# Kernel tuning notes

Measured on AMD Instinct MI355X. Metric: run time of the kernel, lower is better.

Reference implementation:

```python
import jax, jax.numpy as jnp
import numpy as np

DIM, DFF, NH = 768, 2048, 12
HD = DIM // NH
N, NOBJ, L = 16, 52, 24
EPS = 1e-5


def setup_inputs() -> dict:
    key = jax.random.key(0)
    ks = jax.random.split(key, 16)
    g = lambda k, shape: jax.random.normal(k, shape, jnp.float32) * 0.02
    inp = {
        "lang": jax.random.normal(ks[0], (N, L, DIM), jnp.float32),
        "obj": jax.random.normal(ks[1], (N, NOBJ, DIM), jnp.float32),
        "lang_mask": jnp.ones((N, L), jnp.int32),
        "obj_mask": jnp.ones((N, NOBJ), jnp.int32),
        "co_mask": jnp.ones((N, L, NOBJ), jnp.int32),
    }
    # two multi-head attention blocks (edge / node): q,k,v,o projections
    for i, nm in enumerate(["e_wq", "e_wk", "e_wv", "e_wo", "n_wq", "n_wk", "n_wv", "n_wo"]):
        inp[nm] = g(ks[2 + i], (DIM, DIM))
        inp[nm.replace("w", "b")] = jnp.zeros((DIM,), jnp.float32)
    inp["ffn_w1"] = g(ks[10], (2 * DIM, DFF)); inp["ffn_b1"] = jnp.zeros((DFF,), jnp.float32)
    inp["ffn_w2"] = g(ks[11], (DFF, DIM)); inp["ffn_b2"] = jnp.zeros((DIM,), jnp.float32)
    for nm in ["ln_e", "ln_q", "ln2"]:
        inp[nm + "_g"] = jnp.ones((DIM,), jnp.float32)
        inp[nm + "_b"] = jnp.zeros((DIM,), jnp.float32)
    return inp


def _layernorm(x, g, b):
    m = jnp.mean(x, -1, keepdims=True)
    v = jnp.mean((x - m) ** 2, -1, keepdims=True)
    return (x - m) * jax.lax.rsqrt(v + EPS) * g + b


def _fwd(lang, obj, co_mask,
         e_wq, e_bq, e_wk, e_bk, e_wv, e_bv, e_wo, e_bo,
         n_wq, n_bq, n_wk, n_bk, n_wv, n_bv, n_wo, n_bo,
         ffn_w1, ffn_b1, ffn_w2, ffn_b2,
         ln_e_g, ln_e_b, ln_q_g, ln_q_b, ln2_g, ln2_b):
    scale = jnp.float32(1.0 / np.sqrt(HD))
    co_t = co_mask.swapaxes(1, 2)  # [N, nobj, L]: query objects attend over lang keys

    # ---- node branch: standard cross-attention obj -> lang ----
    qh = (obj @ n_wq + n_bq).reshape(N, NOBJ, NH, HD)
    kh = (lang @ n_wk + n_bk).reshape(N, L, NH, HD)
    vh = (lang @ n_wv + n_bv).reshape(N, L, NH, HD)
    s = jnp.einsum('nqhd,nlhd->nhql', qh, kh) * scale  # [N,H,nobj,L]
    s = jnp.where(co_t[:, None, :, :] > 0, s, jnp.float32(-1e9))
    a = jax.nn.softmax(s, axis=-1)
    node = jnp.einsum('nhql,nlhd->nqhd', a, vh).reshape(N, NOBJ, DIM) @ n_wo + n_bo

    # ---- edge branch: pairwise diffs attend over lang, then max over partner ----
    diff = obj[:, :, None, :] - obj[:, None, :, :]            # [N,i,j,D]
    qhe = (diff @ e_wq + e_bq).reshape(N, NOBJ, NOBJ, NH, HD)
    khe = (lang @ e_wk + e_bk).reshape(N, L, NH, HD)
    vhe = (lang @ e_wv + e_bv).reshape(N, L, NH, HD)
    se = jnp.einsum('nijhd,nlhd->nhijl', qhe, khe) * scale    # [N,H,i,j,L]
    # mask depends on (n, j, l): torch repeats co_mask^T over the i batch dim
    se = jnp.where(co_t[:, None, None, :, :] > 0, se, jnp.float32(-1e9))
    ae = jax.nn.softmax(se, axis=-1)
    oe = jnp.einsum('nhijl,nlhd->nijhd', ae, vhe).reshape(N, NOBJ, NOBJ, DIM)
    oe = oe @ e_wo + e_bo                                      # [N,i,j,D]
    edge = jnp.max(oe, axis=2)                                 # max over query/partner j -> [N,i,D]

    # ---- fuse ----
    xe = _layernorm(obj + edge, ln_e_g, ln_e_b)
    xn = _layernorm(obj + node, ln_q_g, ln_q_b)
    h = jnp.concatenate((xn, xe), -1)
    h = jax.nn.relu(h @ ffn_w1 + ffn_b1) @ ffn_w2 + ffn_b2
    return _layernorm(xn + h, ln2_g, ln2_b)


def reference(lang, obj, lang_mask, obj_mask, co_mask,
              e_wq, e_bq, e_wk, e_bk, e_wv, e_bv, e_wo, e_bo,
              n_wq, n_bq, n_wk, n_bk, n_wv, n_bv, n_wo, n_bo,
              ffn_w1, ffn_b1, ffn_w2, ffn_b2,
              ln_e_g, ln_e_b, ln_q_g, ln_q_b, ln2_g, ln2_b):
    return _fwd(lang, obj, co_mask,
                e_wq, e_bq, e_wk, e_bk, e_wv, e_bv, e_wo, e_bo,
                n_wq, n_bq, n_wk, n_bk, n_wv, n_bv, n_wo, n_bo,
                ffn_w1, ffn_b1, ffn_w2, ffn_b2,
                ln_e_g, ln_e_b, ln_q_g, ln_q_b, ln2_g, ln2_b)
```

## Files before the change

kernel.cpp:

```cpp
#include <hip/hip_runtime.h>
#include <math.h>

#define NOBJ 52
#define LL 24
#define NHEAD 12

typedef __attribute__((ext_vector_type(8))) short bf16x8;
typedef __attribute__((ext_vector_type(4))) float f32x4;
typedef __attribute__((ext_vector_type(4))) unsigned int u32x4;
typedef __attribute__((ext_vector_type(2))) unsigned int u32x2;

__device__ __forceinline__ unsigned short f2b(float x) {
    union { float f; unsigned int u; } v; v.f = x;
    unsigned int r = v.u + 0x7fffu + ((v.u >> 16) & 1u);
    return (unsigned short)(r >> 16);
}
__device__ __forceinline__ float b2f(unsigned short u) {
    union { unsigned int u; float f; } v; v.u = ((unsigned int)u) << 16;
    return v.f;
}
__device__ __forceinline__ unsigned int pack2(float a, float b) {
    return (unsigned int)f2b(a) | ((unsigned int)f2b(b) << 16);
}
__device__ __forceinline__ f32x4 mfma16(bf16x8 a, bf16x8 b, f32x4 c) {
    return __builtin_amdgcn_mfma_f32_16x16x32_bf16(a, b, c, 0, 0, 0);
}
__device__ __forceinline__ void gl_lds16(const void* g, void* lds) {
    __builtin_amdgcn_global_load_lds(
        (const __attribute__((address_space(1))) unsigned int*)g,
        (__attribute__((address_space(3))) unsigned int*)lds, 16, 0, 0);
}

__device__ __forceinline__ void transpose_tile(const float* __restrict__ src,
    unsigned short* __restrict__ dst, int K, int N, int t, char* smem)
{
    float (*ts)[65] = (float(*)[65])smem;
    const int tid = threadIdx.x;
    const int ntk = K >> 6;
    const int k0 = (t % ntk) << 6, n0 = (t / ntk) << 6;
    const int tx = tid & 63, ty = tid >> 6;
    #pragma unroll
    for (int i2 = 0; i2 < 16; ++i2) {
        const int row = i2 * 4 + ty;
        ts[row][tx] = src[(size_t)(k0 + row) * N + n0 + tx];
    }
    __syncthreads();
    #pragma unroll
    for (int i2 = 0; i2 < 16; ++i2) {
        const int row = i2 * 4 + ty;
        dst[(size_t)(n0 + row) * K + k0 + tx] = f2b(ts[tx][row]);
    }
}

__global__ __launch_bounds__(256)
void pack_all_kernel(const float* s0, const float* s1, const float* s2,
                     const float* s3, const float* s4, const float* s5,
                     const float* s6, const float* s7,
                     const float* s8, const float* s9,
                     unsigned short* d0, unsigned short* d1, unsigned short* d2,
                     unsigned short* d3, unsigned short* d4, unsigned short* d5,
                     unsigned short* d6, unsigned short* d7,
                     unsigned short* d8, unsigned short* d9,
                     const float* obj, const float* lang, const float* n_bq,
                     const float* e_bk, const float* e_bv,
                     const float* n_bk, const float* n_bv,
                     unsigned short* objb, unsigned short* langb,
                     float* bqc, float* blc)
{
    __shared__ __align__(16) char smem[16640];
    const int bid = blockIdx.x;
    const int tid = threadIdx.x;
    if (bid < 2304) {
        const float* src; unsigned short* dst; int K, N, t;
        if (bid < 1152) {
            const int job = bid / 144; t = bid % 144; K = 768; N = 768;
            switch (job) {
                case 0: src = s0; dst = d0; break;
                case 1: src = s1; dst = d1; break;
                case 2: src = s2; dst = d2; break;
                case 3: src = s3; dst = d3; break;
                case 4: src = s4; dst = d4; break;
                case 5: src = s5; dst = d5; break;
                case 6: src = s6; dst = d6; break;
                default: src = s7; dst = d7; break;
            }
        } else if (bid < 1920) { t = bid - 1152; K = 1536; N = 2048; src = s8; dst = d8; }
        else                   { t = bid - 1920; K = 2048; N = 768;  src = s9; dst = d9; }
        transpose_tile(src, dst, K, N, t, smem);
    } else {
        const int base = ((bid - 2304) * 256 + tid) * 4;
        const int T0 = 638976, T1 = 933888, T2 = 935424, T3 = 938496;
        if (base >= T3) return;
        if (base < T0) {
            f32x4 v = *(const f32x4*)(obj + base);
            *(u32x2*)(objb + base) = (u32x2){pack2(v[0], v[1]), pack2(v[2], v[3])};
        } else if (base < T1) {
            const int j = base - T0;
            f32x4 v = *(const f32x4*)(lang + j);
            *(u32x2*)(langb + j) = (u32x2){pack2(v[0], v[1]), pack2(v[2], v[3])};
        } else if (base < T2) {
            const int j = base - T1;
            if (j < 768) { *(f32x4*)(bqc + j) = (f32x4){0.f, 0.f, 0.f, 0.f}; }
            else         { *(f32x4*)(bqc + j) = *(const f32x4*)(n_bq + j - 768); }
        } else {
            const int j = base - T2;
            const int s = j / 768, c = j % 768;
            const float* p = (s == 0) ? e_bk : (s == 1) ? e_bv : (s == 2) ? n_bk : n_bv;
            *(f32x4*)(blc + j) = *(const f32x4*)(p + c);
        }
    }
}

struct GemmJob {
    const unsigned short* A; const unsigned short* Bt; const float* bias;
    float* C; unsigned short* Cb;
    int lda, ldc, K, nbx, nb, relu, swz;
};

__device__ __forceinline__ void gemm_body(const GemmJob J, int bid, char* smem)
{
    unsigned short* As = (unsigned short*)smem;
    unsigned short* Bs = (unsigned short*)(smem + 16384);
    int bx, by;
    if (J.swz) {
        const int cpx = J.nb >> 3;
        const int gid = (bid & 7) * cpx + (bid >> 3);
        const int nbm = J.nb / J.nbx;
        bx = gid / nbm; by = gid % nbm;
    } else { bx = bid % J.nbx; by = bid / J.nbx; }
    const int n0 = bx * 128, m0 = by * 64;
    const int tid = threadIdx.x;
    const int lane = tid & 63;
    const int w = tid >> 6, wr = w >> 1, wc = w & 1;
    const int lr = lane & 15, lk = lane >> 4;
    const int lda = J.lda, K = J.K;
    const unsigned short* Ab = J.A + (size_t)m0 * lda;
    const unsigned short* Bb = J.Bt + (size_t)n0 * K;

    f32x4 acc[2][4] = {};
    const int NT = K >> 6;

    #pragma unroll
    for (int q = 0; q < 2; ++q) {
        const int c = q * 256 + tid, row = c >> 3, p = (c & 7) ^ (row & 7);
        gl_lds16(Ab + (size_t)row * lda + p * 8, As + c * 8);
    }
    #pragma unroll
    for (int q = 0; q < 4; ++q) {
        const int c = q * 256 + tid, row = c >> 3, p = (c & 7) ^ (row & 7);
        gl_lds16(Bb + (size_t)row * K + p * 8, Bs + c * 8);
    }
    __syncthreads();

    for (int t = 0; t < NT; ++t) {
        const int cur = t & 1;
        if (t + 1 < NT) {
            const int k0 = (t + 1) << 6;
            #pragma unroll
            for (int q = 0; q < 2; ++q) {
                const int c = q * 256 + tid, row = c >> 3, p = (c & 7) ^ (row & 7);
                gl_lds16(Ab + (size_t)row * lda + k0 + p * 8, As + (cur ^ 1) * 4096 + c * 8);
            }
            #pragma unroll
            for (int q = 0; q < 4; ++q) {
                const int c = q * 256 + tid, row = c >> 3, p = (c & 7) ^ (row & 7);
                gl_lds16(Bb + (size_t)row * K + k0 + p * 8, Bs + (cur ^ 1) * 8192 + c * 8);
            }
        }
        #pragma unroll
        for (int kk = 0; kk < 2; ++kk) {
            bf16x8 af[2], bv[4];
            #pragma unroll
            for (int mt = 0; mt < 2; ++mt) {
                const int row = wr * 32 + mt * 16 + lr;
                const int pc = (kk * 4 + lk) ^ (row & 7);
                af[mt] = *(const bf16x8*)(As + cur * 4096 + row * 64 + pc * 8);
            }
            #pragma unroll
            for (int nt = 0; nt < 4; ++nt) {
                const int col = wc * 64 + nt * 16 + lr;
                const int pc = (kk * 4 + lk) ^ (col & 7);
                bv[nt] = *(const bf16x8*)(Bs + cur * 8192 + col * 64 + pc * 8);
            }
            #pragma unroll
            for (int mt = 0; mt < 2; ++mt)
                #pragma unroll
                for (int nt = 0; nt < 4; ++nt)
                    acc[mt][nt] = mfma16(af[mt], bv[nt], acc[mt][nt]);
        }
        __syncthreads();
    }

    #pragma unroll
    for (int mt = 0; mt < 2; ++mt) {
        #pragma unroll
        for (int nt = 0; nt < 4; ++nt) {
            const int col = n0 + wc * 64 + nt * 16 + lr;
            const float bvv = J.bias ? J.bias[col] : 0.f;
            #pragma unroll
            for (int r = 0; r < 4; ++r) {
                const int row = m0 + wr * 32 + mt * 16 + lk * 4 + r;
                float v = acc[mt][nt][r] + bvv;
                if (J.relu) v = fmaxf(v, 0.f);
                if (J.C)  J.C[(size_t)row * J.ldc + col] = v;
                if (J.Cb) J.Cb[(size_t)row * J.ldc + col] = f2b(v);
            }
        }
    }
}

__global__ __launch_bounds__(256)
void gemm_tn(GemmJob j0, GemmJob j1)
{
    __shared__ __align__(16) char smem[49152];
    const int bid = blockIdx.x;
    if (bid < j0.nb) gemm_body(j0, bid, smem);
    else gemm_body(j1, bid - j0.nb, smem);
}

__global__ __launch_bounds__(256)
void mid3_kernel(const unsigned short* __restrict__ QCb,
                 const unsigned short* __restrict__ LCb,
                 const unsigned short* __restrict__ Wet,
                 const unsigned short* __restrict__ Wot,
                 const float* __restrict__ e_bq,
                 unsigned short* __restrict__ VWe,
                 unsigned short* __restrict__ VWn,
                 float* __restrict__ S2e, float* __restrict__ Tb,
                 float* __restrict__ S2n)
{
    __shared__ __align__(16) union USm {
        struct { unsigned short As[8192], Bs[8192]; } g;
        unsigned short Ct[128 * 136];
        struct { float sA[52][68], sB[24][68]; } s;
    } U;
    const int bid = blockIdx.x;
    const int tid = threadIdx.x;

    if (bid < 432) {
        const int sub = bid >= 216;
        const int b = sub ? bid - 216 : bid;
        const int aoff = sub ? 2304 : 768;
        const unsigned short* Bt = sub ? Wot : Wet;
        unsigned short* Vout = sub ? VWn : VWe;

        const int h = b / 18, rm = b % 18, mt = rm / 6, ntile = rm % 6;
        const int m0 = mt * 128, n0 = ntile * 128;
        const int lane = tid & 63, w = tid >> 6, wr = w >> 1, wc = w & 1;
        const int lr = lane & 15, lk = lane >> 4;
        #pragma unroll
        for (int q = 0; q < 4; ++q) {
            const int c = q * 256 + tid, row = c >> 3, p = (c & 7) ^ (row & 7);
            gl_lds16(LCb + (size_t)(m0 + row) * 3072 + aoff + h * 64 + p * 8, &U.g.As[c * 8]);
            gl_lds16(Bt + (size_t)(n0 + row) * 768 + h * 64 + p * 8, &U.g.Bs[c * 8]);
        }
        __syncthreads();
        f32x4 acc[4][4] = {};
        #pragma unroll
        for (int kk = 0; kk < 2; ++kk) {
            bf16x8 af[4], bv[4];
            #pragma unroll
            for (int m2 = 0; m2 < 4; ++m2) {
                const int row = wr * 64 + m2 * 16 + lr;
                const int pc = (kk * 4 + lk) ^ (row & 7);
                af[m2] = *(const bf16x8*)&U.g.As[row * 64 + pc * 8];
            }
            #pragma unroll
            for (int n2 = 0; n2 < 4; ++n2) {
                const int col = wc * 64 + n2 * 16 + lr;
                const int pc = (kk * 4 + lk) ^ (col & 7);
                bv[n2] = *(const bf16x8*)&U.g.Bs[col * 64 + pc * 8];
            }
            #pragma unroll
            for (int m2 = 0; m2 < 4; ++m2)
                #pragma unroll
                for (int n2 = 0; n2 < 4; ++n2)
                    acc[m2][n2] = mfma16(af[m2], bv[n2], acc[m2][n2]);
        }
        __syncthreads();
        #pragma unroll
        for (int m2 = 0; m2 < 4; ++m2)
            #pragma unroll
            for (int n2 = 0; n2 < 4; ++n2) {
                const int col = wc * 64 + n2 * 16 + lr;
                #pragma unroll
                for (int r = 0; r < 4; ++r) {
                    const int row = wr * 64 + m2 * 16 + lk * 4 + r;
                    U.Ct[row * 136 + col] = f2b(acc[m2][n2][r]);
                }
            }
        __syncthreads();
        #pragma unroll
        for (int q = 0; q < 8; ++q) {
            const int item = q * 256 + tid;
            const int dl = item & 127, kg = item >> 7;
            const int m = m0 + kg * 8;
            const int nn = m / 24, l0 = m % 24;
            const int kc = (h * 24 + l0) >> 3;
            const int ks = kc >> 2;
            const int dg = n0 + dl;
            const int kpos = (kc & 3) ^ ((dg >> 1) & 3);
            u32x4 uu;
            #pragma unroll
            for (int e = 0; e < 4; ++e)
                uu[e] = (unsigned int)U.Ct[(kg * 8 + 2 * e) * 136 + dl]
                      | ((unsigned int)U.Ct[(kg * 8 + 2 * e + 1) * 136 + dl] << 16);
            *(u32x4*)(Vout + (size_t)nn * 221184 + ks * 24576 + dg * 32 + kpos * 8) = uu;
        }
    } else {
        const int sub = bid >= 624;
        const int b = bid - (sub ? 624 : 432);
        const int n = b / NHEAD, h = b % NHEAD;
        const int qoff = sub ? 768 : 0, koff = sub ? 1536 : 0;
        float* Sout = sub ? S2n : S2e;
        for (int p = tid; p < 52 * 64; p += 256) {
            const int q = p >> 6, d = p & 63;
            U.s.sA[q][d] = b2f(QCb[(size_t)(n * 52 + q) * 1536 + qoff + h * 64 + d]);
        }
        for (int p = tid; p < 24 * 64; p += 256) {
            const int l = p >> 6, d = p & 63;
            U.s.sB[l][d] = b2f(LCb[(size_t)(n * 24 + l) * 3072 + koff + h * 64 + d]);
        }
        __syncthreads();
        for (int p = tid; p < 52 * 24; p += 256) {
            const int q = p / 24, l = p % 24;
            float s = 0.f;
            #pragma unroll
            for (int d = 0; d < 64; ++d) s += U.s.sA[q][d] * U.s.sB[l][d];
            Sout[((size_t)(n * NHEAD + h) * 52 + q) * 24 + l] = s;
        }
        if (!sub && tid < 24) {
            float s = 0.f;
            #pragma unroll
            for (int d = 0; d < 64; ++d) s += e_bq[h * 64 + d] * U.s.sB[tid][d];
            Tb[((size_t)n * NHEAD + h) * 24 + tid] = s;
        }
    }
}

__global__ __launch_bounds__(256)
void sm_kernel(const float* __restrict__ S2e, const float* __restrict__ Tb,
               const float* __restrict__ S2n, const int* __restrict__ co_mask,
               unsigned short* __restrict__ Pe, unsigned short* __restrict__ Pn)
{
    __shared__ __align__(16) unsigned short Ps[52 * 288];
    __shared__ float SiT[288];
    __shared__ unsigned char cmb[1248];
    const int bid = blockIdx.x;
    const int tid = threadIdx.x;

    if (bid < 832) {
        const int n = bid / 52, i = bid % 52;
        const float* S2x = S2e + (size_t)n * NHEAD * 52 * 24;
        for (int p = tid; p < 288; p += 256) {
            const int h = p / 24, l = p % 24;
            SiT[p] = S2x[((size_t)h * 52 + i) * 24 + l] + Tb[((size_t)n * NHEAD + h) * 24 + l];
        }
        for (int p = tid; p < 1248; p += 256)
            cmb[p] = (unsigned char)(co_mask[(size_t)n * 1248 + p] > 0);
        __syncthreads();
        for (int p = tid; p < 624; p += 256) {
            const int h = p / 52, j = p % 52;
            const float* Sj = S2x + ((size_t)h * 52 + j) * 24;
            const float* st = SiT + h * 24;
            float x[24]; float mx = -1e30f;
            #pragma unroll
            for (int l = 0; l < 24; ++l) {
                float v = (st[l] - Sj[l]) * 0.125f;
                v = cmb[l * 52 + j] ? v : -1e9f;
                x[l] = v; mx = fmaxf(mx, v);
            }
            float sum = 0.f;
            #pragma unroll
            for (int l = 0; l < 24; ++l) { const float e = __expf(x[l] - mx); x[l] = e; sum += e; }
            const float inv = 1.f / sum;
            u32x4* dst = (u32x4*)(Ps + j * 288 + h * 24);
            u32x4 u0, u1, u2;
            #pragma unroll
            for (int c = 0; c < 4; ++c) {
                u0[c] = pack2(x[2 * c] * inv, x[2 * c + 1] * inv);
                u1[c] = pack2(x[8 + 2 * c] * inv, x[9 + 2 * c] * inv);
                u2[c] = pack2(x[16 + 2 * c] * inv, x[17 + 2 * c] * inv);
            }
            dst[0] = u0; dst[1] = u1; dst[2] = u2;
        }
        __syncthreads();
        unsigned short* dstG = Pe + (size_t)bid * 14976;
        for (int p = tid; p < 1872; p += 256)
            *(u32x4*)(dstG + p * 8) = *(const u32x4*)(Ps + p * 8);
    } else {
        const int n = bid - 832;
        const float* S2x = S2n + (size_t)n * NHEAD * 52 * 24;
        for (int p = tid; p < 1248; p += 256)
            cmb[p] = (unsigned char)(co_mask[(size_t)n * 1248 + p] > 0);
        __syncthreads();
        for (int p = tid; p < 624; p += 256) {
            const int h = p / 52, q = p % 52;
            const float* Sq = S2x + ((size_t)h * 52 + q) * 24;
            float x[24]; float mx = -1e30f;
            #pragma unroll
            for (int l = 0; l < 24; ++l) {
                float v = Sq[l] * 0.125f;
                v = cmb[l * 52 + q] ? v : -1e9f;
                x[l] = v; mx = fmaxf(mx, v);
            }
            float sum = 0.f;
            #pragma unroll
            for (int l = 0; l < 24; ++l) { const float e = __expf(x[l] - mx); x[l] = e; sum += e; }
            const float inv = 1.f / sum;
            u32x4* dst = (u32x4*)(Ps + q * 288 + h * 24);
            u32x4 u0, u1, u2;
            #pragma unroll
            for (int c = 0; c < 4; ++c) {
                u0[c] = pack2(x[2 * c] * inv, x[2 * c + 1] * inv);
                u1[c] = pack2(x[8 + 2 * c] * inv, x[9 + 2 * c] * inv);
                u2[c] = pack2(x[16 + 2 * c] * inv, x[17 + 2 * c] * inv);
            }
            dst[0] = u0; dst[1] = u1; dst[2] = u2;
        }
        __syncthreads();
        unsigned short* dstG = Pn + (size_t)n * 14976;
        for (int p = tid; p < 1872; p += 256)
            *(u32x4*)(dstG + p * 8) = *(const u32x4*)(Ps + p * 8);
    }
}

__global__ __launch_bounds__(256)
void av_kernel(const unsigned short* __restrict__ Pe,
               const unsigned short* __restrict__ Pn,
               const unsigned short* __restrict__ VWe,
               const unsigned short* __restrict__ VWn,
               const float* __restrict__ ebo, const float* __restrict__ nbo,
               unsigned short* __restrict__ EdgeBb,
               unsigned short* __restrict__ NodePb)
{
    __shared__ __align__(16) char smem[40960];
    unsigned short* As = (unsigned short*)smem;
    unsigned short* Bs = (unsigned short*)(smem + 16384);
    const int bid = blockIdx.x;
    const int tid = threadIdx.x;
    const int lane = tid & 63, w = tid >> 6;
    const int lr = lane & 15, lk = lane >> 4;

    if (bid < 1664) {
        const int sw = (bid & 7) * 208 + (bid >> 3);
        const int n = sw / 104;
        const int r104 = sw % 104;
        const int ip = r104 >> 2, dq = r104 & 3;
        const int i0 = ip * 2;
        const unsigned short* Pa = Pe + (size_t)(n * 52 + i0) * 14976;
        const unsigned short* Bsrc = VWe + (size_t)n * 221184 + dq * 6144;

        const int ca0 = tid, ca1 = 256 + tid;
        const int ro0 = (ca0 >> 2) & 63, kp0 = ca0 & 3;
        const int ro1 = (ca1 >> 2) & 63, kp1 = ca1 & 3;
        const int sa0 = (ca0 >> 8) * 14976 + ro0 * 288 + ((kp0 ^ ((ro0 >> 1) & 3)) << 3);
        const int sa1 = (ca1 >> 8) * 14976 + ro1 * 288 + ((kp1 ^ ((ro1 >> 1) & 3)) << 3);

        gl_lds16(Pa + sa0, As + ca0 * 8);
        gl_lds16(Pa + sa1, As + ca1 * 8);
        #pragma unroll
        for (int q = 0; q < 3; ++q) {
            const int c = q * 256 + tid;
            gl_lds16(Bsrc + c * 8, Bs + c * 8);
        }
        __syncthreads();

        const int iw = w >> 1, cg = (w & 1) * 96;
        f32x4 acc[4][6] = {};
        for (int ks = 0; ks < 9; ++ks) {
            const int cur = ks & 1;
            if (ks < 8) {
                const int nb = cur ^ 1;
                gl_lds16(Pa + sa0 + (ks + 1) * 32, As + nb * 4096 + ca0 * 8);
                gl_lds16(Pa + sa1 + (ks + 1) * 32, As + nb * 4096 + ca1 * 8);
                #pragma unroll
                for (int q = 0; q < 3; ++q) {
                    const int c = q * 256 + tid;
                    gl_lds16(Bsrc + (size_t)(ks + 1) * 24576 + c * 8, Bs + nb * 6144 + c * 8);
                }
            }
            bf16x8 af[4];
            #pragma unroll
            for (int mt = 0; mt < 4; ++mt) {
                const int row = mt * 16 + lr;
                af[mt] = *(const bf16x8*)(As + cur * 4096 + iw * 2048 + row * 32
                                          + ((lk ^ ((row >> 1) & 3)) << 3));
            }
            #pragma unroll
            for (int nt = 0; nt < 6; ++nt) {
                const int cl = cg + nt * 16 + lr;
                bf16x8 bv = *(const bf16x8*)(Bs + cur * 6144 + cl * 32
                                             + ((lk ^ ((cl >> 1) & 3)) << 3));
                #pragma unroll
                for (int mt = 0; mt < 4; ++mt)
                    acc[mt][nt] = mfma16(af[mt], bv, acc[mt][nt]);
            }
            __syncthreads();
        }

        #pragma unroll
        for (int nt = 0; nt < 6; ++nt) {
            float m = -1e30f;
            #pragma unroll
            for (int mt = 0; mt < 4; ++mt)
                #pragma unroll
                for (int r = 0; r < 4; ++r) {
                    const int row = mt * 16 + lk * 4 + r;
                    if (row < NOBJ) m = fmaxf(m, acc[mt][nt][r]);
                }
            m = fmaxf(m, __shfl_xor(m, 16));
            m = fmaxf(m, __shfl_xor(m, 32));
            if (lk == 0) {
                const int col = dq * 192 + cg + nt * 16 + lr;
                EdgeBb[(size_t)(n * 52 + i0 + iw) * 768 + col] = f2b(m + ebo[col]);
            }
        }
    } else {
        const int t = bid - 1664;
        const int n = t >> 2, dq = t & 3;
        const unsigned short* Pa = Pn + (size_t)n * 14976;
        const unsigned short* Bsrc = VWn + (size_t)n * 221184 + dq * 6144;

        const int ro = (tid >> 2) & 63, kp = tid & 3;
        const int sa = ro * 288 + ((kp ^ ((ro >> 1) & 3)) << 3);

        gl_lds16(Pa + sa, As + tid * 8);
        #pragma unroll
        for (int q = 0; q < 3; ++q) {
            const int c = q * 256 + tid;
            gl_lds16(Bsrc + c * 8, Bs + c * 8);
        }
        __syncthreads();

        const int cg = w * 48;
        f32x4 acc[4][3] = {};
        for (int ks = 0; ks < 9; ++ks) {
            const int cur = ks & 1;
            if (ks < 8) {
                const int nb = cur ^ 1;
                gl_lds16(Pa + sa + (ks + 1) * 32, As + nb * 4096 + tid * 8);
                #pragma unroll
                for (int q = 0; q < 3; ++q) {
                    const int c = q * 256 + tid;
                    gl_lds16(Bsrc + (size_t)(ks + 1) * 24576 + c * 8, Bs + nb * 6144 + c * 8);
                }
            }
            bf16x8 af[4];
            #pragma unroll
            for (int mt = 0; mt < 4; ++mt) {
                const int row = mt * 16 + lr;
                af[mt] = *(const bf16x8*)(As + cur * 4096 + row * 32
                                          + ((lk ^ ((row >> 1) & 3)) << 3));
            }
            #pragma unroll
            for (int nt = 0; nt < 3; ++nt) {
                const int cl = cg + nt * 16 + lr;
                bf16x8 bv = *(const bf16x8*)(Bs + cur * 6144 + cl * 32
                                             + ((lk ^ ((cl >> 1) & 3)) << 3));
                #pragma unroll
                for (int mt = 0; mt < 4; ++mt)
                    acc[mt][nt] = mfma16(af[mt], bv, acc[mt][nt]);
            }
            __syncthreads();
        }

        #pragma unroll
        for (int nt = 0; nt < 3; ++nt) {
            const int col = dq * 192 + cg + nt * 16 + lr;
            const float bv = nbo[col];
            #pragma unroll
            for (int mt = 0; mt < 4; ++mt)
                #pragma unroll
                for (int r = 0; r < 4; ++r) {
                    const int row = mt * 16 + lk * 4 + r;
                    if (row < NOBJ)
                        NodePb[(size_t)(n * 52 + row) * 768 + col] = f2b(acc[mt][nt][r] + bv);
                }
        }
    }
}

__global__ __launch_bounds__(256)
void ln_dual_kernel(const float* __restrict__ obj,
                    const unsigned short* __restrict__ NodePb,
                    const unsigned short* __restrict__ EdgeBb,
                    const float* __restrict__ gq, const float* __restrict__ bq,
                    const float* __restrict__ ge, const float* __restrict__ be,
                    unsigned short* __restrict__ Fusedb)
{
    __shared__ float red[8];
    const int job = blockIdx.x >= 832;
    const int row = blockIdx.x - (job ? 832 : 0);
    const int tid = threadIdx.x;
    const unsigned short* x2 = (job ? EdgeBb : NodePb) + (size_t)row * 768;
    const float* x1 = obj + (size_t)row * 768;
    const float* g = job ? ge : gq;
    const float* bb = job ? be : bq;
    float v[3]; float s = 0.f;
    #pragma unroll
    for (int c = 0; c < 3; ++c) {
        const int col = tid + 256 * c;
        v[c] = x1[col] + b2f(x2[col]); s += v[c];
    }
    #pragma unroll
    for (int o = 32; o; o >>= 1) s += __shfl_xor(s, o);
    if ((tid & 63) == 0) red[tid >> 6] = s;
    __syncthreads();
    const float mean = (red[0] + red[1] + red[2] + red[3]) * (1.f / 768.f);
    float var = 0.f;
    #pragma unroll
    for (int c = 0; c < 3; ++c) { const float d = v[c] - mean; var += d * d; }
    #pragma unroll
    for (int o = 32; o; o >>= 1) var += __shfl_xor(var, o);
    __syncthreads();
    if ((tid & 63) == 0) red[4 + (tid >> 6)] = var;
    __syncthreads();
    const float vt = (red[4] + red[5] + red[6] + red[7]) * (1.f / 768.f);
    const float rs = rsqrtf(vt + 1e-5f);
    unsigned short* dst = Fusedb + (size_t)row * 1536 + (job ? 768 : 0);
    #pragma unroll
    for (int c = 0; c < 3; ++c) {
        const int col = tid + 256 * c;
        dst[col] = f2b((v[c] - mean) * rs * g[col] + bb[col]);
    }
}

__global__ __launch_bounds__(256)
void ln2_kernel(const unsigned short* __restrict__ x1b,
                const float* __restrict__ x2,
                const float* __restrict__ g, const float* __restrict__ bb,
                float* __restrict__ dst)
{
    __shared__ float red[8];
    const int row = blockIdx.x, tid = threadIdx.x;
    float v[3]; float s = 0.f;
    #pragma unroll
    for (int c = 0; c < 3; ++c) {
        const int col = tid + 256 * c;
        v[c] = b2f(x1b[(size_t)row * 1536 + col]) + x2[(size_t)row * 768 + col];
        s += v[c];
    }
    #pragma unroll
    for (int o = 32; o; o >>= 1) s += __shfl_xor(s, o);
    if ((tid & 63) == 0) red[tid >> 6] = s;
    __syncthreads();
    const float mean = (red[0] + red[1] + red[2] + red[3]) * (1.f / 768.f);
    float var = 0.f;
    #pragma unroll
    for (int c = 0; c < 3; ++c) { const float d = v[c] - mean; var += d * d; }
    #pragma unroll
    for (int o = 32; o; o >>= 1) var += __shfl_xor(var, o);
    __syncthreads();
    if ((tid & 63) == 0) red[4 + (tid >> 6)] = var;
    __syncthreads();
    const float vt = (red[4] + red[5] + red[6] + red[7]) * (1.f / 768.f);
    const float rs = rsqrtf(vt + 1e-5f);
    #pragma unroll
    for (int c = 0; c < 3; ++c) {
        const int col = tid + 256 * c;
        dst[(size_t)row * 768 + col] = (v[c] - mean) * rs * g[col] + bb[col];
    }
}

extern "C" void kernel_launch(void* const* d_in, const int* in_sizes, int n_in,
                              void* d_out, int out_size, void* d_ws, size_t ws_size,
                              hipStream_t stream)
{
    (void)in_sizes; (void)n_in; (void)out_size; (void)ws_size;
    const float* lang  = (const float*)d_in[0];
    const float* obj   = (const float*)d_in[1];
    const int* co_mask = (const int*)d_in[4];
    const float* e_wq = (const float*)d_in[5];
    const float* e_bq = (const float*)d_in[6];
    const float* e_wk = (const float*)d_in[7];
    const float* e_bk = (const float*)d_in[8];
    const float* e_wv = (const float*)d_in[9];
    const float* e_bv = (const float*)d_in[10];
    const float* e_wo = (const float*)d_in[11];
    const float* e_bo = (const float*)d_in[12];
    const float* n_wq = (const float*)d_in[13];
    const float* n_bq = (const float*)d_in[14];
    const float* n_wk = (const float*)d_in[15];
    const float* n_bk = (const float*)d_in[16];
    const float* n_wv = (const float*)d_in[17];
    const float* n_bv = (const float*)d_in[18];
    const float* n_wo = (const float*)d_in[19];
    const float* n_bo = (const float*)d_in[20];
    const float* ffn_w1 = (const float*)d_in[21];
    const float* ffn_b1 = (const float*)d_in[22];
    const float* ffn_w2 = (const float*)d_in[23];
    const float* ffn_b2 = (const float*)d_in[24];
    const float* ln_e_g = (const float*)d_in[25];
    const float* ln_e_b = (const float*)d_in[26];
    const float* ln_q_g = (const float*)d_in[27];
    const float* ln_q_b = (const float*)d_in[28];
    const float* ln2_g = (const float*)d_in[29];
    const float* ln2_b = (const float*)d_in[30];
    float* out = (float*)d_out;

    char* wsb = (char*)d_ws;
    unsigned short* Wqt   = (unsigned short*)(wsb + 0);
    unsigned short* Wlt   = (unsigned short*)(wsb + 2359296);
    unsigned short* Wet   = (unsigned short*)(wsb + 7077888);
    unsigned short* Wot   = (unsigned short*)(wsb + 8257536);
    unsigned short* W1t   = (unsigned short*)(wsb + 9437184);
    unsigned short* W2t   = (unsigned short*)(wsb + 15728640);
    unsigned short* objb  = (unsigned short*)(wsb + 18874368);
    unsigned short* langb = (unsigned short*)(wsb + 20152320);
    float*          bqc   = (float*)(wsb + 20742144);
    float*          blc   = (float*)(wsb + 20748288);
    unsigned short* QCb   = (unsigned short*)(wsb + 20760576);
    unsigned short* LCb   = (unsigned short*)(wsb + 23316480);
    float*          S2e   = (float*)(wsb + 25675776);
    float*          Tb    = (float*)(wsb + 26634240);
    float*          S2n   = (float*)(wsb + 26652672);
    unsigned short* VWe   = (unsigned short*)(wsb + 27611136);
    unsigned short* VWn   = (unsigned short*)(wsb + 34689024);
    unsigned short* Pe    = (unsigned short*)(wsb + 41766912);
    unsigned short* Pn    = (unsigned short*)(wsb + 66686976);
    unsigned short* NodePb= (unsigned short*)(wsb + 67198976);
    unsigned short* EdgeBb= (unsigned short*)(wsb + 68476928);
    unsigned short* Fusedb= (unsigned short*)(wsb + 69754880);
    unsigned short* H1b   = (unsigned short*)(wsb + 72310784);
    float*          H2    = (float*)(wsb + 75718656);

    dim3 blk(256);
    pack_all_kernel<<<3221, blk, 0, stream>>>(
        e_wq, n_wq, e_wk, e_wv, n_wk, n_wv, n_wo, e_wo, ffn_w1, ffn_w2,
        Wqt, Wqt + 589824, Wlt, Wlt + 589824, Wlt + 2 * 589824, Wlt + 3 * 589824,
        Wot, Wet, W1t, W2t,
        obj, lang, n_bq, e_bk, e_bv, n_bk, n_bv, objb, langb, bqc, blc);
    {
        GemmJob p0 = {objb, Wqt, bqc, nullptr, QCb, 768, 1536, 768, 12, 156, 0, 0};
        GemmJob p1 = {langb, Wlt, blc, nullptr, LCb, 768, 3072, 768, 24, 144, 0, 0};
        gemm_tn<<<300, blk, 0, stream>>>(p0, p1);
    }
    mid3_kernel<<<816, blk, 0, stream>>>(QCb, LCb, Wet, Wot, e_bq,
                                         VWe, VWn, S2e, Tb, S2n);
    sm_kernel<<<848, blk, 0, stream>>>(S2e, Tb, S2n, co_mask, Pe, Pn);
    av_kernel<<<1728, blk, 0, stream>>>(Pe, Pn, VWe, VWn, e_bo, n_bo, EdgeBb, NodePb);
    ln_dual_kernel<<<1664, blk, 0, stream>>>(obj, NodePb, EdgeBb, ln_q_g, ln_q_b,
                                             ln_e_g, ln_e_b, Fusedb);
    {
        GemmJob p0 = {Fusedb, W1t, ffn_b1, nullptr, H1b, 1536, 2048, 1536, 16, 208, 1, 1};
        gemm_tn<<<208, blk, 0, stream>>>(p0, p0);
    }
    {
        GemmJob p0 = {H1b, W2t, ffn_b2, H2, nullptr, 2048, 768, 2048, 6, 78, 0, 0};
        gemm_tn<<<78, blk, 0, stream>>>(p0, p0);
    }
    ln2_kernel<<<832, blk, 0, stream>>>(Fusedb, H2, ln2_g, ln2_b, out);
}
```

Measured before the change: 137.7 us.

## Split-K the FFN down-projection and overlap FFN weight packing with projections

```diff
diff --git a/kernel.cpp b/kernel.cpp
--- a/kernel.cpp
+++ b/kernel.cpp
@@ -53,42 +53,37 @@
 }
 
 __global__ __launch_bounds__(256)
-void pack_all_kernel(const float* s0, const float* s1, const float* s2,
-                     const float* s3, const float* s4, const float* s5,
-                     const float* s6, const float* s7,
-                     const float* s8, const float* s9,
-                     unsigned short* d0, unsigned short* d1, unsigned short* d2,
-                     unsigned short* d3, unsigned short* d4, unsigned short* d5,
-                     unsigned short* d6, unsigned short* d7,
-                     unsigned short* d8, unsigned short* d9,
-                     const float* obj, const float* lang, const float* n_bq,
-                     const float* e_bk, const float* e_bv,
-                     const float* n_bk, const float* n_bv,
-                     unsigned short* objb, unsigned short* langb,
-                     float* bqc, float* blc)
+void pack1_kernel(const float* s0, const float* s1, const float* s2,
+                  const float* s3, const float* s4, const float* s5,
+                  const float* s6, const float* s7,
+                  unsigned short* d0, unsigned short* d1, unsigned short* d2,
+                  unsigned short* d3, unsigned short* d4, unsigned short* d5,
+                  unsigned short* d6, unsigned short* d7,
+                  const float* obj, const float* lang, const float* n_bq,
+                  const float* e_bk, const float* e_bv,
+                  const float* n_bk, const float* n_bv,
+                  unsigned short* objb, unsigned short* langb,
+                  float* bqc, float* blc)
 {
     __shared__ __align__(16) char smem[16640];
     const int bid = blockIdx.x;
     const int tid = threadIdx.x;
-    if (bid < 2304) {
-        const float* src; unsigned short* dst; int K, N, t;
-        if (bid < 1152) {
-            const int job = bid / 144; t = bid % 144; K = 768; N = 768;
-            switch (job) {
-                case 0: src = s0; dst = d0; break;
-                case 1: src = s1; dst = d1; break;
-                case 2: src = s2; dst = d2; break;
-                case 3: src = s3; dst = d3; break;
-                case 4: src = s4; dst = d4; break;
-                case 5: src = s5; dst = d5; break;
-                case 6: src = s6; dst = d6; break;
-                default: src = s7; dst = d7; break;
-            }
-        } else if (bid < 1920) { t = bid - 1152; K = 1536; N = 2048; src = s8; dst = d8; }
-        else                   { t = bid - 1920; K = 2048; N = 768;  src = s9; dst = d9; }
-        transpose_tile(src, dst, K, N, t, smem);
+    if (bid < 1152) {
+        const int job = bid / 144, t = bid % 144;
+        const float* src; unsigned short* dst;
+        switch (job) {
+            case 0: src = s0; dst = d0; break;
+            case 1: src = s1; dst = d1; break;
+            case 2: src = s2; dst = d2; break;
+            case 3: src = s3; dst = d3; break;
+            case 4: src = s4; dst = d4; break;
+            case 5: src = s5; dst = d5; break;
+            case 6: src = s6; dst = d6; break;
+            default: src = s7; dst = d7; break;
+        }
+        transpose_tile(src, dst, 768, 768, t, smem);
     } else {
-        const int base = ((bid - 2304) * 256 + tid) * 4;
+        const int base = ((bid - 1152) * 256 + tid) * 4;
         const int T0 = 638976, T1 = 933888, T2 = 935424, T3 = 938496;
         if (base >= T3) return;
         if (base < T0) {
@@ -114,7 +109,7 @@
 struct GemmJob {
     const unsigned short* A; const unsigned short* Bt; const float* bias;
     float* C; unsigned short* Cb;
-    int lda, ldc, K, nbx, nb, relu, swz;
+    int lda, ldb, ldc, K, nbx, nb, relu, swz;
 };
 
 __device__ __forceinline__ void gemm_body(const GemmJob J, int bid, char* smem)
@@ -133,9 +128,9 @@
     const int lane = tid & 63;
     const int w = tid >> 6, wr = w >> 1, wc = w & 1;
     const int lr = lane & 15, lk = lane >> 4;
-    const int lda = J.lda, K = J.K;
+    const int lda = J.lda, ldb = J.ldb, K = J.K;
     const unsigned short* Ab = J.A + (size_t)m0 * lda;
-    const unsigned short* Bb = J.Bt + (size_t)n0 * K;
+    const unsigned short* Bb = J.Bt + (size_t)n0 * ldb;
 
     f32x4 acc[2][4] = {};
     const int NT = K >> 6;
@@ -148,7 +143,7 @@
     #pragma unroll
     for (int q = 0; q < 4; ++q) {
         const int c = q * 256 + tid, row = c >> 3, p = (c & 7) ^ (row & 7);
-        gl_lds16(Bb + (size_t)row * K + p * 8, Bs + c * 8);
+        gl_lds16(Bb + (size_t)row * ldb + p * 8, Bs + c * 8);
     }
     __syncthreads();
 
@@ -164,7 +159,7 @@
             #pragma unroll
             for (int q = 0; q < 4; ++q) {
                 const int c = q * 256 + tid, row = c >> 3, p = (c & 7) ^ (row & 7);
-                gl_lds16(Bb + (size_t)row * K + k0 + p * 8, Bs + (cur ^ 1) * 8192 + c * 8);
+                gl_lds16(Bb + (size_t)row * ldb + k0 + p * 8, Bs + (cur ^ 1) * 8192 + c * 8);
             }
         }
         #pragma unroll
@@ -210,12 +205,32 @@
 }
 
 __global__ __launch_bounds__(256)
-void gemm_tn(GemmJob j0, GemmJob j1)
+void gemm_tn4(GemmJob j0, GemmJob j1, GemmJob j2, GemmJob j3)
 {
     __shared__ __align__(16) char smem[49152];
-    const int bid = blockIdx.x;
-    if (bid < j0.nb) gemm_body(j0, bid, smem);
-    else gemm_body(j1, bid - j0.nb, smem);
+    int bid = blockIdx.x;
+    if (bid < j0.nb) { gemm_body(j0, bid, smem); return; }
+    bid -= j0.nb;
+    if (bid < j1.nb) { gemm_body(j1, bid, smem); return; }
+    bid -= j1.nb;
+    if (bid < j2.nb) { gemm_body(j2, bid, smem); return; }
+    bid -= j2.nb;
+    gemm_body(j3, bid, smem);
+}
+
+__global__ __launch_bounds__(256)
+void proj_pack_kernel(GemmJob j0, GemmJob j1,
+                      const float* w1, const float* w2,
+                      unsigned short* W1t, unsigned short* W2t)
+{
+    __shared__ __align__(16) char smem[49152];
+    int bid = blockIdx.x;
+    if (bid < j0.nb) { gemm_body(j0, bid, smem); return; }
+    bid -= j0.nb;
+    if (bid < j1.nb) { gemm_body(j1, bid, smem); return; }
+    const int t = bid - j1.nb;
+    if (t < 768) transpose_tile(w1, W1t, 1536, 2048, t, smem);
+    else transpose_tile(w2, W2t, 2048, 768, t - 768, smem);
 }
 
 __global__ __launch_bounds__(256)
@@ -628,7 +643,7 @@
 
 __global__ __launch_bounds__(256)
 void ln2_kernel(const unsigned short* __restrict__ x1b,
-                const float* __restrict__ x2,
+                const float* __restrict__ Hp, const float* __restrict__ b2,
                 const float* __restrict__ g, const float* __restrict__ bb,
                 float* __restrict__ dst)
 {
@@ -638,7 +653,9 @@
     #pragma unroll
     for (int c = 0; c < 3; ++c) {
         const int col = tid + 256 * c;
-        v[c] = b2f(x1b[(size_t)row * 1536 + col]) + x2[(size_t)row * 768 + col];
+        const size_t o = (size_t)row * 768 + col;
+        float h = Hp[o] + Hp[638976 + o] + Hp[2 * 638976 + o] + Hp[3 * 638976 + o];
+        v[c] = b2f(x1b[(size_t)row * 1536 + col]) + h + b2[col];
         s += v[c];
     }
     #pragma unroll
@@ -723,18 +740,18 @@
     unsigned short* EdgeBb= (unsigned short*)(wsb + 68476928);
     unsigned short* Fusedb= (unsigned short*)(wsb + 69754880);
     unsigned short* H1b   = (unsigned short*)(wsb + 72310784);
-    float*          H2    = (float*)(wsb + 75718656);
+    float*          Hp    = (float*)(wsb + 75718656);
 
     dim3 blk(256);
-    pack_all_kernel<<<3221, blk, 0, stream>>>(
-        e_wq, n_wq, e_wk, e_wv, n_wk, n_wv, n_wo, e_wo, ffn_w1, ffn_w2,
+    pack1_kernel<<<2069, blk, 0, stream>>>(
+        e_wq, n_wq, e_wk, e_wv, n_wk, n_wv, n_wo, e_wo,
         Wqt, Wqt + 589824, Wlt, Wlt + 589824, Wlt + 2 * 589824, Wlt + 3 * 589824,
-        Wot, Wet, W1t, W2t,
+        Wot, Wet,
         obj, lang, n_bq, e_bk, e_bv, n_bk, n_bv, objb, langb, bqc, blc);
     {
-        GemmJob p0 = {objb, Wqt, bqc, nullptr, QCb, 768, 1536, 768, 12, 156, 0, 0};
-        GemmJob p1 = {langb, Wlt, blc, nullptr, LCb, 768, 3072, 768, 24, 144, 0, 0};
-        gemm_tn<<<300, blk, 0, stream>>>(p0, p1);
+        GemmJob p0 = {objb, Wqt, bqc, nullptr, QCb, 768, 768, 1536, 768, 12, 156, 0, 0};
+        GemmJob p1 = {langb, Wlt, blc, nullptr, LCb, 768, 768, 3072, 768, 24, 144, 0, 0};
+        proj_pack_kernel<<<1452, blk, 0, stream>>>(p0, p1, ffn_w1, ffn_w2, W1t, W2t);
     }
     mid3_kernel<<<816, blk, 0, stream>>>(QCb, LCb, Wet, Wot, e_bq,
                                          VWe, VWn, S2e, Tb, S2n);
@@ -743,12 +760,15 @@
     ln_dual_kernel<<<1664, blk, 0, stream>>>(obj, NodePb, EdgeBb, ln_q_g, ln_q_b,
                                              ln_e_g, ln_e_b, Fusedb);
     {
-        GemmJob p0 = {Fusedb, W1t, ffn_b1, nullptr, H1b, 1536, 2048, 1536, 16, 208, 1, 1};
-        gemm_tn<<<208, blk, 0, stream>>>(p0, p0);
+        GemmJob p0 = {Fusedb, W1t, ffn_b1, nullptr, H1b, 1536, 1536, 2048, 1536, 16, 208, 1, 1};
+        gemm_tn4<<<208, blk, 0, stream>>>(p0, p0, p0, p0);
     }
     {
-        GemmJob p0 = {H1b, W2t, ffn_b2, H2, nullptr, 2048, 768, 2048, 6, 78, 0, 0};
-        gemm_tn<<<78, blk, 0, stream>>>(p0, p0);
-    }
-    ln2_kernel<<<832, blk, 0, stream>>>(Fusedb, H2, ln2_g, ln2_b, out);
-}
+        GemmJob q0 = {H1b,        W2t,        nullptr, Hp,               nullptr, 2048, 2048, 768, 512, 6, 78, 0, 0};
+        GemmJob q1 = {H1b + 512,  W2t + 512,  nullptr, Hp + 638976,      nullptr, 2048, 2048, 768, 512, 6, 78, 0, 0};
+        GemmJob q2 = {H1b + 1024, W2t + 1024, nullptr, Hp + 2 * 638976,  nullptr, 2048, 2048, 768, 512, 6, 78, 0, 0};
+        GemmJob q3 = {H1b + 1536, W2t + 1536, nullptr, Hp + 3 * 638976,  nullptr, 2048, 2048, 768, 512, 6, 78, 0, 0};
+        gemm_tn4<<<312, blk, 0, stream>>>(q0, q1, q2, q3);
+    }
+    ln2_kernel<<<832, blk, 0, stream>>>(Fusedb, Hp, ffn_b2, ln2_g, ln2_b, out);
+}
```

Result: faster. 125.2 us (-9.1%).
